# Kernel tuning notes

Measured on AMD Instinct MI355X. Metric: run time of the kernel, lower is better.

Reference implementation:

```python
import jax, jax.numpy as jnp
import numpy as np

NUM_USERS = 100000
NUM_ITEMS = 50000
N_NODES = NUM_USERS + NUM_ITEMS
EMBED_DIM = 64
N_LAYERS = 3
NNZ = 4000000


def setup_inputs() -> dict:
    key = jax.random.key(0)
    k1, k2, k3, k4, k5 = jax.random.split(key, 5)
    # Xavier-uniform-ish embedding tables (exact init distribution irrelevant for correctness)
    user_emb = jax.random.normal(k1, (NUM_USERS, EMBED_DIM), dtype=jnp.float32) * 0.1
    item_emb = jax.random.normal(k2, (NUM_ITEMS, EMBED_DIM), dtype=jnp.float32) * 0.1
    # Sparse normalized adjacency in COO form; scale values like a degree-normalized graph
    vals = jax.random.uniform(k3, (NNZ,), dtype=jnp.float32) * 0.02
    rows = jax.random.randint(k4, (NNZ,), 0, N_NODES, dtype=jnp.int32)
    cols = jax.random.randint(k5, (NNZ,), 0, N_NODES, dtype=jnp.int32)
    return {"user_emb": user_emb, "item_emb": item_emb, "vals": vals,
            "rows": rows, "cols": cols}


def _spmm(vals, rows, cols, x):
    # out[r] = sum_{e: rows[e]==r} vals[e] * x[cols[e]]  -- COO SpMM
    return jax.ops.segment_sum(vals[:, None] * x[cols], rows, num_segments=N_NODES)


def reference(user_emb, item_emb, vals, rows, cols):
    all_emb = jnp.concatenate([user_emb, item_emb], axis=0)  # [N, D]
    emb_sum = all_emb
    h = all_emb
    for _ in range(N_LAYERS):
        h = _spmm(vals, rows, cols, h)
        emb_sum = emb_sum + h
    final = emb_sum / jnp.float32(N_LAYERS + 1)  # mean over layer stack
    users = final[:NUM_USERS]
    items = final[NUM_USERS:]
    return users, items
```

## Files before the change

### kernel.cpp

```cpp
#include <hip/hip_runtime.h>
#include <hip/hip_bf16.h>


#define NUSERS 100000
#define NITEMS 50000
#define NNODES 150000
#define DIM    64
#define NNZ_E  4000000
#define BSH    9
#define NBKT   ((NNODES + 511) / 512)
#define CHUNK  8192
#define NB1    ((NNZ_E + CHUNK - 1) / CHUNK)

__device__ inline unsigned short f2b(float f) {
    __hip_bfloat16 h = __float2bfloat16(f);
    return *reinterpret_cast<unsigned short*>(&h);
}
__device__ inline float b2f(unsigned short b) {
    return __uint_as_float((unsigned)b << 16);
}


__global__ void bhist_k(const int* __restrict__ rows, int* __restrict__ bcnt) {
    __shared__ int cnt[NBKT];
    for (int i = threadIdx.x; i < NBKT; i += 256) cnt[i] = 0;
    __syncthreads();
    int stride = gridDim.x * 256;
    for (int i = blockIdx.x * 256 + threadIdx.x; i < NNZ_E; i += stride)
        atomicAdd(&cnt[rows[i] >> BSH], 1);
    __syncthreads();
    for (int i = threadIdx.x; i < NBKT; i += 256)
        if (cnt[i]) atomicAdd(&bcnt[i], cnt[i]);
}


__global__ void bscan_k(const int* __restrict__ bcnt, int* __restrict__ bbase,
                        int* __restrict__ bcur, int* __restrict__ rs) {
    __shared__ int s[512];
    int t = threadIdx.x;
    int v = (t < NBKT) ? bcnt[t] : 0;
    s[t] = v;
    __syncthreads();
    for (int off = 1; off < 512; off <<= 1) {
        int add = (t >= off) ? s[t - off] : 0;
        __syncthreads();
        s[t] += add;
        __syncthreads();
    }
    if (t < NBKT) {
        int ex = s[t] - v;
        bbase[t] = ex;
        bcur[t]  = ex;
    }
    if (t == 0) {
        bbase[NBKT] = NNZ_E;
        rs[NNODES]  = NNZ_E;
    }
}


__global__ void pass1_k(const int* __restrict__ rows, const int* __restrict__ cols,
                        const float* __restrict__ vals, int* __restrict__ bcur,
                        int2* __restrict__ ebuf) {
    __shared__ int lcnt[NBKT];
    __shared__ int lcur[NBKT];
    int base = blockIdx.x * CHUNK;
    int end  = min(base + CHUNK, NNZ_E);
    for (int i = threadIdx.x; i < NBKT; i += 256) lcnt[i] = 0;
    __syncthreads();
    for (int i = base + threadIdx.x; i < end; i += 256)
        atomicAdd(&lcnt[rows[i] >> BSH], 1);
    __syncthreads();
    for (int i = threadIdx.x; i < NBKT; i += 256)
        lcur[i] = lcnt[i] ? atomicAdd(&bcur[i], lcnt[i]) : 0;
    __syncthreads();
    for (int i = base + threadIdx.x; i < end; i += 256) {
        int r = rows[i];
        int p = atomicAdd(&lcur[r >> BSH], 1);
        ebuf[p] = make_int2(cols[i] | ((r & 511) << 18), __float_as_int(vals[i]));
    }
}


__global__ void passC_k(const int* __restrict__ bbase, const int2* __restrict__ ebuf,
                        int* __restrict__ rs, int2* __restrict__ cedge) {
    __shared__ int rcnt[512];
    __shared__ int rbase[512];
    __shared__ int s[256];
    int b  = blockIdx.x;
    int t  = threadIdx.x;
    int s0 = bbase[b], e0 = bbase[b + 1];
    int rows0 = b << BSH;
    int nrows = min(512, NNODES - rows0);

    rcnt[t] = 0; rcnt[t + 256] = 0;
    __syncthreads();
    for (int j = s0 + t; j < e0; j += 256)
        atomicAdd(&rcnt[(unsigned)ebuf[j].x >> 18], 1);
    __syncthreads();

    int a0 = rcnt[2 * t], a1 = rcnt[2 * t + 1];
    s[t] = a0 + a1;
    __syncthreads();
    for (int off = 1; off < 256; off <<= 1) {
        int add = (t >= off) ? s[t - off] : 0;
        __syncthreads();
        s[t] += add;
        __syncthreads();
    }
    int pbase = s[t] - (a0 + a1);
    rbase[2 * t]     = pbase;
    rbase[2 * t + 1] = pbase + a0;
    __syncthreads();

    if (t < nrows)           rs[rows0 + t]       = s0 + rbase[t];
    if (t + 256 < nrows)     rs[rows0 + t + 256] = s0 + rbase[t + 256];

    rcnt[t] = rbase[t]; rcnt[t + 256] = rbase[t + 256];
    __syncthreads();

    for (int j = s0 + t; j < e0; j += 256) {
        int2 ee = ebuf[j];
        int lr  = (unsigned)ee.x >> 18;
        int pos = s0 + atomicAdd(&rcnt[lr], 1);
        cedge[pos] = make_int2(ee.x & 0x3FFFF, ee.y);
    }
}


__global__ void init_k(const float4* __restrict__ ue, const float4* __restrict__ ie,
                       ushort4* __restrict__ h0, float4* __restrict__ esum) {
    int i = blockIdx.x * 256 + threadIdx.x;
    const int NU4 = NUSERS * (DIM / 4);
    const int NT4 = NNODES * (DIM / 4);
    if (i < NT4) {
        float4 v = (i < NU4) ? ue[i] : ie[i - NU4];
        esum[i] = v;
        ushort4 b;
        b.x = f2b(v.x); b.y = f2b(v.y); b.z = f2b(v.z); b.w = f2b(v.w);
        h0[i] = b;
    }
}


template <int FINAL>
__global__ void spmm_k(const int* __restrict__ rs, const int2* __restrict__ cedge,
                       const unsigned short* __restrict__ x,
                       unsigned short* __restrict__ hout, float* __restrict__ esum) {
    int pair = (blockIdx.x * blockDim.x + threadIdx.x) >> 6;
    int lane = threadIdx.x & 63;
    int half = lane >> 5;
    int m    = lane & 31;
    int row  = pair * 2 + half;
    if (row >= NNODES) return;
    int s = rs[row], e = rs[row + 1];
    const char* xb = (const char*)x;

    float acc0 = 0.f, acc1 = 0.f;
    int j = s;
    for (; j + 8 <= e; j += 8) {
        int2 e0 = cedge[j],     e1 = cedge[j + 1];
        int2 e2 = cedge[j + 2], e3 = cedge[j + 3];
        int2 e4 = cedge[j + 4], e5 = cedge[j + 5];
        int2 e6 = cedge[j + 6], e7 = cedge[j + 7];
        unsigned u0 = *(const unsigned*)(xb + ((size_t)e0.x << 7) + (m << 2));
        unsigned u1 = *(const unsigned*)(xb + ((size_t)e1.x << 7) + (m << 2));
        unsigned u2 = *(const unsigned*)(xb + ((size_t)e2.x << 7) + (m << 2));
        unsigned u3 = *(const unsigned*)(xb + ((size_t)e3.x << 7) + (m << 2));
        unsigned u4 = *(const unsigned*)(xb + ((size_t)e4.x << 7) + (m << 2));
        unsigned u5 = *(const unsigned*)(xb + ((size_t)e5.x << 7) + (m << 2));
        unsigned u6 = *(const unsigned*)(xb + ((size_t)e6.x << 7) + (m << 2));
        unsigned u7 = *(const unsigned*)(xb + ((size_t)e7.x << 7) + (m << 2));
        float v0 = __int_as_float(e0.y), v1 = __int_as_float(e1.y);
        float v2 = __int_as_float(e2.y), v3 = __int_as_float(e3.y);
        float v4 = __int_as_float(e4.y), v5 = __int_as_float(e5.y);
        float v6 = __int_as_float(e6.y), v7 = __int_as_float(e7.y);
        acc0 = fmaf(v0, __uint_as_float(u0 << 16), acc0);
        acc1 = fmaf(v0, __uint_as_float(u0 & 0xffff0000u), acc1);
        acc0 = fmaf(v1, __uint_as_float(u1 << 16), acc0);
        acc1 = fmaf(v1, __uint_as_float(u1 & 0xffff0000u), acc1);
        acc0 = fmaf(v2, __uint_as_float(u2 << 16), acc0);
        acc1 = fmaf(v2, __uint_as_float(u2 & 0xffff0000u), acc1);
        acc0 = fmaf(v3, __uint_as_float(u3 << 16), acc0);
        acc1 = fmaf(v3, __uint_as_float(u3 & 0xffff0000u), acc1);
        acc0 = fmaf(v4, __uint_as_float(u4 << 16), acc0);
        acc1 = fmaf(v4, __uint_as_float(u4 & 0xffff0000u), acc1);
        acc0 = fmaf(v5, __uint_as_float(u5 << 16), acc0);
        acc1 = fmaf(v5, __uint_as_float(u5 & 0xffff0000u), acc1);
        acc0 = fmaf(v6, __uint_as_float(u6 << 16), acc0);
        acc1 = fmaf(v6, __uint_as_float(u6 & 0xffff0000u), acc1);
        acc0 = fmaf(v7, __uint_as_float(u7 << 16), acc0);
        acc1 = fmaf(v7, __uint_as_float(u7 & 0xffff0000u), acc1);
    }
    for (; j < e; ++j) {
        int2 ee = cedge[j];
        unsigned u = *(const unsigned*)(xb + ((size_t)ee.x << 7) + (m << 2));
        float v = __int_as_float(ee.y);
        acc0 = fmaf(v, __uint_as_float(u << 16), acc0);
        acc1 = fmaf(v, __uint_as_float(u & 0xffff0000u), acc1);
    }

    int o2 = row * 32 + m;
    float2 rv = ((const float2*)esum)[o2];
    float r0 = rv.x + acc0, r1 = rv.y + acc1;
    if (FINAL) {
        ((float2*)esum)[o2] = make_float2(r0 * 0.25f, r1 * 0.25f);
    } else {
        ((float2*)esum)[o2] = make_float2(r0, r1);
        ((unsigned*)hout)[o2] = ((unsigned)f2b(acc1) << 16) | f2b(acc0);
    }
}


extern "C" void kernel_launch(void* const* d_in, const int* in_sizes, int n_in,
                              void* d_out, int out_size, void* d_ws, size_t ws_size,
                              hipStream_t stream) {
    const float* ue   = (const float*)d_in[0];
    const float* ie   = (const float*)d_in[1];
    const float* vals = (const float*)d_in[2];
    const int*   rows = (const int*)d_in[3];
    const int*   cols = (const int*)d_in[4];
    float*       out  = (float*)d_out;

    char*  ws  = (char*)d_ws;
    size_t off = 0;
    auto alloc = [&](size_t bytes) -> char* {
        char* p = ws + off;
        off += (bytes + 255) & ~size_t(255);
        return p;
    };
    unsigned short* h0 = (unsigned short*)alloc((size_t)NNODES * DIM * 2);
    unsigned short* h1 = (unsigned short*)alloc((size_t)NNODES * DIM * 2);
    int2*  cedge  = (int2*)alloc((size_t)NNZ_E * 8);
    int2*  ebuf   = (int2*)alloc((size_t)NNZ_E * 8);
    int*   rs     = (int*)alloc((size_t)(NNODES + 1) * 4);
    int*   bcnt   = (int*)alloc((size_t)(NBKT + 1) * 4);
    int*   bbase  = (int*)alloc((size_t)(NBKT + 1) * 4);
    int*   bcur   = (int*)alloc((size_t)(NBKT + 1) * 4);
    (void)in_sizes; (void)n_in; (void)out_size;

    if (ws_size < off) return;

    hipMemsetAsync(bcnt, 0, (size_t)(NBKT + 1) * 4, stream);
    bhist_k<<<256, 256, 0, stream>>>(rows, bcnt);
    bscan_k<<<1, 512, 0, stream>>>(bcnt, bbase, bcur, rs);
    pass1_k<<<NB1, 256, 0, stream>>>(rows, cols, vals, bcur, ebuf);
    passC_k<<<NBKT, 256, 0, stream>>>(bbase, ebuf, rs, cedge);

    init_k<<<(NNODES * (DIM / 4) + 255) / 256, 256, 0, stream>>>(
        (const float4*)ue, (const float4*)ie, (ushort4*)h0, (float4*)out);

    const int SG = (NNODES / 2) * 64 / 256;
    spmm_k<0><<<SG, 256, 0, stream>>>(rs, cedge, h0, h1, out);
    spmm_k<0><<<SG, 256, 0, stream>>>(rs, cedge, h1, h0, out);
    spmm_k<1><<<SG, 256, 0, stream>>>(rs, cedge, h0, h1, out);
}
```

Measured before the change: 554.8 us.

## Fuse init into histogram, halve bucket size, unroll SpMM gather by 16

Merges the embedding init/bf16 conversion into the bucket histogram kernel, removing one launch. Bucket size drops from 512 to 256 rows, so the partition kernel gets twice as many blocks and a simpler one-row-per-thread scan, while the bucket scan now uses 1024 threads. The SpMM inner loop is unrolled to 16 gathers in flight, with an 8-wide remainder step, to raise memory-level parallelism at the cost of more registers. The fused init runs on only 256 blocks, which may be slower than the old full-grid init.

```diff
diff --git a/kernel.cpp b/kernel.cpp
--- a/kernel.cpp
+++ b/kernel.cpp
@@ -7,8 +7,8 @@
 #define NNODES 150000
 #define DIM    64
 #define NNZ_E  4000000
-#define BSH    9
-#define NBKT   ((NNODES + 511) / 512)
+#define BSH    8
+#define NBKT   ((NNODES + 255) / 256)
 #define CHUNK  8192
 #define NB1    ((NNZ_E + CHUNK - 1) / CHUNK)
 
@@ -21,27 +21,42 @@
 }
 
 
-__global__ void bhist_k(const int* __restrict__ rows, int* __restrict__ bcnt) {
+__global__ void bhist_k(const int* __restrict__ rows, int* __restrict__ bcnt,
+                        const float4* __restrict__ ue, const float4* __restrict__ ie,
+                        ushort4* __restrict__ h0, float4* __restrict__ esum) {
     __shared__ int cnt[NBKT];
     for (int i = threadIdx.x; i < NBKT; i += 256) cnt[i] = 0;
     __syncthreads();
     int stride = gridDim.x * 256;
-    for (int i = blockIdx.x * 256 + threadIdx.x; i < NNZ_E; i += stride)
+    int tid = blockIdx.x * 256 + threadIdx.x;
+    for (int i = tid; i < NNZ_E; i += stride)
         atomicAdd(&cnt[rows[i] >> BSH], 1);
+
+    const int NU4 = NUSERS * (DIM / 4);
+    const int NT4 = NNODES * (DIM / 4);
+    for (int i = tid; i < NT4; i += stride) {
+        float4 v = (i < NU4) ? ue[i] : ie[i - NU4];
+        esum[i] = v;
+        ushort4 b;
+        b.x = f2b(v.x); b.y = f2b(v.y); b.z = f2b(v.z); b.w = f2b(v.w);
+        h0[i] = b;
+    }
+
     __syncthreads();
     for (int i = threadIdx.x; i < NBKT; i += 256)
         if (cnt[i]) atomicAdd(&bcnt[i], cnt[i]);
 }
 
 
-__global__ void bscan_k(const int* __restrict__ bcnt, int* __restrict__ bbase,
-                        int* __restrict__ bcur, int* __restrict__ rs) {
-    __shared__ int s[512];
+__global__ void __launch_bounds__(1024) bscan_k(const int* __restrict__ bcnt,
+                        int* __restrict__ bbase, int* __restrict__ bcur,
+                        int* __restrict__ rs) {
+    __shared__ int s[1024];
     int t = threadIdx.x;
     int v = (t < NBKT) ? bcnt[t] : 0;
     s[t] = v;
     __syncthreads();
-    for (int off = 1; off < 512; off <<= 1) {
+    for (int off = 1; off < 1024; off <<= 1) {
         int add = (t >= off) ? s[t - off] : 0;
         __syncthreads();
         s[t] += add;
@@ -77,30 +92,29 @@
     for (int i = base + threadIdx.x; i < end; i += 256) {
         int r = rows[i];
         int p = atomicAdd(&lcur[r >> BSH], 1);
-        ebuf[p] = make_int2(cols[i] | ((r & 511) << 18), __float_as_int(vals[i]));
+        ebuf[p] = make_int2(cols[i] | ((r & 255) << 18), __float_as_int(vals[i]));
     }
 }
 
 
 __global__ void passC_k(const int* __restrict__ bbase, const int2* __restrict__ ebuf,
                         int* __restrict__ rs, int2* __restrict__ cedge) {
-    __shared__ int rcnt[512];
-    __shared__ int rbase[512];
+    __shared__ int rcnt[256];
     __shared__ int s[256];
     int b  = blockIdx.x;
     int t  = threadIdx.x;
     int s0 = bbase[b], e0 = bbase[b + 1];
     int rows0 = b << BSH;
-    int nrows = min(512, NNODES - rows0);
-
-    rcnt[t] = 0; rcnt[t + 256] = 0;
+    int nrows = min(256, NNODES - rows0);
+
+    rcnt[t] = 0;
     __syncthreads();
     for (int j = s0 + t; j < e0; j += 256)
         atomicAdd(&rcnt[(unsigned)ebuf[j].x >> 18], 1);
     __syncthreads();
 
-    int a0 = rcnt[2 * t], a1 = rcnt[2 * t + 1];
-    s[t] = a0 + a1;
+    int v = rcnt[t];
+    s[t] = v;
     __syncthreads();
     for (int off = 1; off < 256; off <<= 1) {
         int add = (t >= off) ? s[t - off] : 0;
@@ -108,15 +122,10 @@
         s[t] += add;
         __syncthreads();
     }
-    int pbase = s[t] - (a0 + a1);
-    rbase[2 * t]     = pbase;
-    rbase[2 * t + 1] = pbase + a0;
-    __syncthreads();
-
-    if (t < nrows)           rs[rows0 + t]       = s0 + rbase[t];
-    if (t + 256 < nrows)     rs[rows0 + t + 256] = s0 + rbase[t + 256];
-
-    rcnt[t] = rbase[t]; rcnt[t + 256] = rbase[t + 256];
+    int ex = s[t] - v;
+    if (t < nrows) rs[rows0 + t] = s0 + ex;
+    __syncthreads();
+    rcnt[t] = ex;
     __syncthreads();
 
     for (int j = s0 + t; j < e0; j += 256) {
@@ -124,21 +133,6 @@
         int lr  = (unsigned)ee.x >> 18;
         int pos = s0 + atomicAdd(&rcnt[lr], 1);
         cedge[pos] = make_int2(ee.x & 0x3FFFF, ee.y);
-    }
-}
-
-
-__global__ void init_k(const float4* __restrict__ ue, const float4* __restrict__ ie,
-                       ushort4* __restrict__ h0, float4* __restrict__ esum) {
-    int i = blockIdx.x * 256 + threadIdx.x;
-    const int NU4 = NUSERS * (DIM / 4);
-    const int NT4 = NNODES * (DIM / 4);
-    if (i < NT4) {
-        float4 v = (i < NU4) ? ue[i] : ie[i - NU4];
-        esum[i] = v;
-        ushort4 b;
-        b.x = f2b(v.x); b.y = f2b(v.y); b.z = f2b(v.z); b.w = f2b(v.w);
-        h0[i] = b;
     }
 }
 
@@ -158,46 +152,43 @@
 
     float acc0 = 0.f, acc1 = 0.f;
     int j = s;
-    for (; j + 8 <= e; j += 8) {
-        int2 e0 = cedge[j],     e1 = cedge[j + 1];
-        int2 e2 = cedge[j + 2], e3 = cedge[j + 3];
-        int2 e4 = cedge[j + 4], e5 = cedge[j + 5];
-        int2 e6 = cedge[j + 6], e7 = cedge[j + 7];
-        unsigned u0 = *(const unsigned*)(xb + ((size_t)e0.x << 7) + (m << 2));
-        unsigned u1 = *(const unsigned*)(xb + ((size_t)e1.x << 7) + (m << 2));
-        unsigned u2 = *(const unsigned*)(xb + ((size_t)e2.x << 7) + (m << 2));
-        unsigned u3 = *(const unsigned*)(xb + ((size_t)e3.x << 7) + (m << 2));
-        unsigned u4 = *(const unsigned*)(xb + ((size_t)e4.x << 7) + (m << 2));
-        unsigned u5 = *(const unsigned*)(xb + ((size_t)e5.x << 7) + (m << 2));
-        unsigned u6 = *(const unsigned*)(xb + ((size_t)e6.x << 7) + (m << 2));
-        unsigned u7 = *(const unsigned*)(xb + ((size_t)e7.x << 7) + (m << 2));
-        float v0 = __int_as_float(e0.y), v1 = __int_as_float(e1.y);
-        float v2 = __int_as_float(e2.y), v3 = __int_as_float(e3.y);
-        float v4 = __int_as_float(e4.y), v5 = __int_as_float(e5.y);
-        float v6 = __int_as_float(e6.y), v7 = __int_as_float(e7.y);
-        acc0 = fmaf(v0, __uint_as_float(u0 << 16), acc0);
-        acc1 = fmaf(v0, __uint_as_float(u0 & 0xffff0000u), acc1);
-        acc0 = fmaf(v1, __uint_as_float(u1 << 16), acc0);
-        acc1 = fmaf(v1, __uint_as_float(u1 & 0xffff0000u), acc1);
-        acc0 = fmaf(v2, __uint_as_float(u2 << 16), acc0);
-        acc1 = fmaf(v2, __uint_as_float(u2 & 0xffff0000u), acc1);
-        acc0 = fmaf(v3, __uint_as_float(u3 << 16), acc0);
-        acc1 = fmaf(v3, __uint_as_float(u3 & 0xffff0000u), acc1);
-        acc0 = fmaf(v4, __uint_as_float(u4 << 16), acc0);
-        acc1 = fmaf(v4, __uint_as_float(u4 & 0xffff0000u), acc1);
-        acc0 = fmaf(v5, __uint_as_float(u5 << 16), acc0);
-        acc1 = fmaf(v5, __uint_as_float(u5 & 0xffff0000u), acc1);
-        acc0 = fmaf(v6, __uint_as_float(u6 << 16), acc0);
-        acc1 = fmaf(v6, __uint_as_float(u6 & 0xffff0000u), acc1);
-        acc0 = fmaf(v7, __uint_as_float(u7 << 16), acc0);
-        acc1 = fmaf(v7, __uint_as_float(u7 & 0xffff0000u), acc1);
+    for (; j + 16 <= e; j += 16) {
+        int2 ee[16];
+        unsigned u[16];
+        #pragma unroll
+        for (int k = 0; k < 16; ++k) ee[k] = cedge[j + k];
+        #pragma unroll
+        for (int k = 0; k < 16; ++k)
+            u[k] = *(const unsigned*)(xb + ((size_t)ee[k].x << 7) + (m << 2));
+        #pragma unroll
+        for (int k = 0; k < 16; ++k) {
+            float v = __int_as_float(ee[k].y);
+            acc0 = fmaf(v, __uint_as_float(u[k] << 16), acc0);
+            acc1 = fmaf(v, __uint_as_float(u[k] & 0xffff0000u), acc1);
+        }
+    }
+    if (j + 8 <= e) {
+        int2 ee[8];
+        unsigned u[8];
+        #pragma unroll
+        for (int k = 0; k < 8; ++k) ee[k] = cedge[j + k];
+        #pragma unroll
+        for (int k = 0; k < 8; ++k)
+            u[k] = *(const unsigned*)(xb + ((size_t)ee[k].x << 7) + (m << 2));
+        #pragma unroll
+        for (int k = 0; k < 8; ++k) {
+            float v = __int_as_float(ee[k].y);
+            acc0 = fmaf(v, __uint_as_float(u[k] << 16), acc0);
+            acc1 = fmaf(v, __uint_as_float(u[k] & 0xffff0000u), acc1);
+        }
+        j += 8;
     }
     for (; j < e; ++j) {
         int2 ee = cedge[j];
-        unsigned u = *(const unsigned*)(xb + ((size_t)ee.x << 7) + (m << 2));
+        unsigned uu = *(const unsigned*)(xb + ((size_t)ee.x << 7) + (m << 2));
         float v = __int_as_float(ee.y);
-        acc0 = fmaf(v, __uint_as_float(u << 16), acc0);
-        acc1 = fmaf(v, __uint_as_float(u & 0xffff0000u), acc1);
+        acc0 = fmaf(v, __uint_as_float(uu << 16), acc0);
+        acc1 = fmaf(v, __uint_as_float(uu & 0xffff0000u), acc1);
     }
 
     int o2 = row * 32 + m;
@@ -242,13 +233,11 @@
     if (ws_size < off) return;
 
     hipMemsetAsync(bcnt, 0, (size_t)(NBKT + 1) * 4, stream);
-    bhist_k<<<256, 256, 0, stream>>>(rows, bcnt);
-    bscan_k<<<1, 512, 0, stream>>>(bcnt, bbase, bcur, rs);
+    bhist_k<<<256, 256, 0, stream>>>(rows, bcnt, (const float4*)ue,
+                                     (const float4*)ie, (ushort4*)h0, (float4*)out);
+    bscan_k<<<1, 1024, 0, stream>>>(bcnt, bbase, bcur, rs);
     pass1_k<<<NB1, 256, 0, stream>>>(rows, cols, vals, bcur, ebuf);
     passC_k<<<NBKT, 256, 0, stream>>>(bbase, ebuf, rs, cedge);
-
-    init_k<<<(NNODES * (DIM / 4) + 255) / 256, 256, 0, stream>>>(
-        (const float4*)ue, (const float4*)ie, (ushort4*)h0, (float4*)out);
 
     const int SG = (NNODES / 2) * 64 / 256;
     spmm_k<0><<<SG, 256, 0, stream>>>(rs, cedge, h0, h1, out);
```

Result: slower. 578.7 us (+4.3%).
